# Performance work log

Measured on AMD Instinct MI355X. Metric: run time of the kernel, lower is better.

The kernel has to match this reference:

```python
import jax, jax.numpy as jnp
import numpy as np

IMG = 12
SIZE = 100000
ACC_SCALE = 255.0     # accurate_dft scale
APX_SCALE = 65536.0   # mod_scale for mult index 1 (in {1,2,4,10,11})


def _dft_mat():
    # scipy.linalg.dft(12): W[j,k] = exp(-2*pi*i*j*k/12); module adds 1e-5
    j = np.arange(IMG)
    W = np.exp(-2j * np.pi * np.outer(j, j) / IMG)
    return W.real + 1e-5, W.imag + 1e-5


def setup_inputs() -> dict:
    key = jax.random.key(0)
    x = jax.random.uniform(key, (1, SIZE, IMG, IMG), dtype=jnp.float32) * 255.0
    re, im = _dft_mat()
    wr = jnp.asarray(re.reshape(1, IMG * IMG), dtype=jnp.float32)
    wi = jnp.asarray(im.reshape(1, IMG * IMG), dtype=jnp.float32)
    return {"input": x, "weight_real": wr, "weight_imag": wi}


def _dft_pass(wr_flat, wi_flat, x, scale, rounded):
    # x: (size, 12, 12); wr_flat/wi_flat: (144,)
    rw = wr_flat.reshape(IMG, IMG)
    iw = wi_flat.reshape(IMG, IMG)
    if rounded:  # approx_dft quantizes weights to integers in [-(scale-1), scale-1]
        rw = jnp.round(rw * (scale - 1.0))
        iw = jnp.round(iw * (scale - 1.0))
    else:        # accurate_dft just scales
        rw = rw * scale
        iw = iw * scale
    # approx_matmul's tile/elementwise-mul/group-sum is exactly W @ x[i] per batch
    rt = jnp.matmul(rw, x) / scale          # (size,12,12)
    it = jnp.matmul(iw, x) / scale
    ro = (jnp.matmul(rt, rw) - jnp.matmul(it, iw)) / scale
    io = (jnp.matmul(rt, iw) + jnp.matmul(it, rw)) / scale
    return jnp.sqrt(ro * ro + io * io)      # |re + i*im|


def reference(input, weight_real, weight_imag):
    x = input[:, :, :IMG, :IMG][0]  # (size,12,12)
    acc = _dft_pass(weight_real[0], weight_imag[0], x, ACC_SCALE, False)
    apx = _dft_pass(weight_real[0], weight_imag[0], x, APX_SCALE, True)
    # torch `x.data = x_data` -> straight-through: value = approx, grad via accurate
    out = acc + jax.lax.stop_gradient(apx - acc)
    # output layout [len(mult_list)=1, 1, size, 12, 12]
    return out[None, None]
```

## Files before the change

### kernel.cpp

```cpp
#include <hip/hip_runtime.h>

#define IMG  12
#define NPIX 144
#define IPB  21
#define XSTR 148
#define THREADS 256

__device__ __forceinline__ float rfl(float v) {
    return __builtin_bit_cast(float, __builtin_amdgcn_readfirstlane(__builtin_bit_cast(int, v)));
}

__global__ __launch_bounds__(THREADS)
void dft_apx_kernel(const float* __restrict__ x,
                    const float* __restrict__ wr,
                    const float* __restrict__ wi,
                    float* __restrict__ out, int size)
{
    __shared__ float bufA[IPB * XSTR];
    __shared__ float bufB[IPB * XSTR];

    const int tid  = threadIdx.x;
    const int img0 = blockIdx.x * IPB;
    int nimg = size - img0; if (nimg > IPB) nimg = IPB;

    float cq[12], sq[12];
    #pragma unroll
    for (int m = 0; m < 12; ++m) {
        cq[m] = rfl(rintf(wr[12 + m] * 65535.0f));
        sq[m] = rfl(rintf(wi[12 + m] * 65535.0f));
    }

    const float4* xg = (const float4*)(x + (size_t)img0 * NPIX);
    const int n4 = nimg * (NPIX / 4);
    for (int i = tid; i < n4; i += THREADS) {
        const int im = i / 36, e4 = i % 36;
        *(float4*)&bufA[im * XSTR + e4 * 4] = xg[i];
    }
    __syncthreads();

    const int img_l  = tid / IMG;
    const int lane12 = tid - img_l * IMG;
    const bool active = (tid < IPB * IMG) && (img_l < nimg);

    float xr[12];
    if (active) {
        #pragma unroll
        for (int j = 0; j < 12; ++j)
            xr[j] = bufA[img_l * XSTR + j * IMG + lane12];
    }
    __syncthreads();

    if (active) {
        #pragma unroll
        for (int r = 0; r < 12; ++r) {
            float ar = 0.0f, ai = 0.0f;
            #pragma unroll
            for (int j = 0; j < 12; ++j) {
                const int m = (r * j) % 12;
                ar = fmaf(cq[m], xr[j], ar);
                ai = fmaf(sq[m], xr[j], ai);
            }
            bufA[img_l * XSTR + r * IMG + lane12] = ar;
            bufB[img_l * XSTR + r * IMG + lane12] = ai;
        }
    }
    __syncthreads();

    if (active) {
        float rt[12], it[12];
        #pragma unroll
        for (int q = 0; q < 3; ++q) {
            float4 a = *(const float4*)&bufA[img_l * XSTR + lane12 * IMG + q * 4];
            float4 b = *(const float4*)&bufB[img_l * XSTR + lane12 * IMG + q * 4];
            rt[q*4+0]=a.x; rt[q*4+1]=a.y; rt[q*4+2]=a.z; rt[q*4+3]=a.w;
            it[q*4+0]=b.x; it[q*4+1]=b.y; it[q*4+2]=b.z; it[q*4+3]=b.w;
        }
        const float inv32 = 2.3283064365386963e-10f;
        float o[12];
        #pragma unroll
        for (int cc = 0; cc < 12; ++cc) {
            float ro = 0.0f, io = 0.0f;
            #pragma unroll
            for (int j = 0; j < 12; ++j) {
                const int m = (j * cc) % 12;
                ro = fmaf(rt[j],  cq[m], ro);
                ro = fmaf(-it[j], sq[m], ro);
                io = fmaf(rt[j],  sq[m], io);
                io = fmaf(it[j],  cq[m], io);
            }
            o[cc] = __builtin_amdgcn_sqrtf(fmaf(ro, ro, io * io)) * inv32;
        }
        float4* og = (float4*)(out + (size_t)(img0 + img_l) * NPIX + lane12 * IMG);
        og[0] = make_float4(o[0], o[1], o[2],  o[3]);
        og[1] = make_float4(o[4], o[5], o[6],  o[7]);
        og[2] = make_float4(o[8], o[9], o[10], o[11]);
    }
}

extern "C" void kernel_launch(void* const* d_in, const int* in_sizes, int n_in,
                              void* d_out, int out_size, void* d_ws, size_t ws_size,
                              hipStream_t stream) {
    const float* x  = (const float*)d_in[0];
    const float* wr = (const float*)d_in[1];
    const float* wi = (const float*)d_in[2];
    float* out = (float*)d_out;

    const int size = in_sizes[0] / NPIX;
    const int blocks = (size + IPB - 1) / IPB;
    dft_apx_kernel<<<blocks, THREADS, 0, stream>>>(x, wr, wi, out, size);
}
```

Measured before the change: 125.0 us.

## Map one image per thread with register-held input and shared weight table

Changes the work decomposition from 12 threads per image with LDS transposes to one thread per image. Each thread holds the whole 144-float image in registers and computes each output row directly. The quantized, index-permuted weights go into a small shared table read as float4 broadcasts. This removes the LDS staging buffers and the intermediate barriers, but needs a very large register footprint per thread, and each thread's float4 loads are strided 576 bytes from its neighbours, so global accesses are poorly coalesced.

```diff
diff --git a/kernel.cpp b/kernel.cpp
--- a/kernel.cpp
+++ b/kernel.cpp
@@ -2,98 +2,89 @@
 
 #define IMG  12
 #define NPIX 144
-#define IPB  21
-#define XSTR 148
-#define THREADS 256
+#define THREADS 64
 
 __device__ __forceinline__ float rfl(float v) {
     return __builtin_bit_cast(float, __builtin_amdgcn_readfirstlane(__builtin_bit_cast(int, v)));
 }
 
-__global__ __launch_bounds__(THREADS)
+__global__ __launch_bounds__(THREADS, 2)
 void dft_apx_kernel(const float* __restrict__ x,
                     const float* __restrict__ wr,
                     const float* __restrict__ wi,
                     float* __restrict__ out, int size)
 {
-    __shared__ float bufA[IPB * XSTR];
-    __shared__ float bufB[IPB * XSTR];
+    __shared__ float wqc[NPIX], wqs[NPIX];
 
-    const int tid  = threadIdx.x;
-    const int img0 = blockIdx.x * IPB;
-    int nimg = size - img0; if (nimg > IPB) nimg = IPB;
+    const int tid = threadIdx.x;
+    for (int t = tid; t < NPIX; t += THREADS) {
+        const int r = t / IMG, j = t - r * IMG;
+        const int m = (r * j) % IMG;
+        wqc[t] = rintf(wr[IMG + m] * 65535.0f);
+        wqs[t] = rintf(wi[IMG + m] * 65535.0f);
+    }
+    __syncthreads();
 
     float cq[12], sq[12];
     #pragma unroll
     for (int m = 0; m < 12; ++m) {
-        cq[m] = rfl(rintf(wr[12 + m] * 65535.0f));
-        sq[m] = rfl(rintf(wi[12 + m] * 65535.0f));
+        cq[m] = rfl(rintf(wr[IMG + m] * 65535.0f));
+        sq[m] = rfl(rintf(wi[IMG + m] * 65535.0f));
     }
 
-    const float4* xg = (const float4*)(x + (size_t)img0 * NPIX);
-    const int n4 = nimg * (NPIX / 4);
-    for (int i = tid; i < n4; i += THREADS) {
-        const int im = i / 36, e4 = i % 36;
-        *(float4*)&bufA[im * XSTR + e4 * 4] = xg[i];
+    const int img = blockIdx.x * THREADS + tid;
+    if (img >= size) return;
+
+    float X[NPIX];
+    const float4* xg = (const float4*)(x + (size_t)img * NPIX);
+    #pragma unroll
+    for (int k = 0; k < NPIX / 4; ++k) {
+        const float4 v = xg[k];
+        X[4*k+0] = v.x; X[4*k+1] = v.y; X[4*k+2] = v.z; X[4*k+3] = v.w;
     }
-    __syncthreads();
 
-    const int img_l  = tid / IMG;
-    const int lane12 = tid - img_l * IMG;
-    const bool active = (tid < IPB * IMG) && (img_l < nimg);
+    float* og = out + (size_t)img * NPIX;
+    const float inv32 = 2.3283064365386963e-10f;
 
-    float xr[12];
-    if (active) {
+    #pragma unroll 1
+    for (int r = 0; r < IMG; ++r) {
+        float cr[12], sr[12];
         #pragma unroll
-        for (int j = 0; j < 12; ++j)
-            xr[j] = bufA[img_l * XSTR + j * IMG + lane12];
-    }
-    __syncthreads();
-
-    if (active) {
+        for (int q = 0; q < 3; ++q) {
+            const float4 a = *(const float4*)&wqc[r * IMG + 4*q];
+            const float4 b = *(const float4*)&wqs[r * IMG + 4*q];
+            cr[4*q+0]=a.x; cr[4*q+1]=a.y; cr[4*q+2]=a.z; cr[4*q+3]=a.w;
+            sr[4*q+0]=b.x; sr[4*q+1]=b.y; sr[4*q+2]=b.z; sr[4*q+3]=b.w;
+        }
+        float rt[12], it[12];
         #pragma unroll
-        for (int r = 0; r < 12; ++r) {
-            float ar = 0.0f, ai = 0.0f;
+        for (int c = 0; c < 12; ++c) {
+            float a = 0.0f, b = 0.0f;
             #pragma unroll
             for (int j = 0; j < 12; ++j) {
-                const int m = (r * j) % 12;
-                ar = fmaf(cq[m], xr[j], ar);
-                ai = fmaf(sq[m], xr[j], ai);
+                a = fmaf(cr[j], X[j*12 + c], a);
+                b = fmaf(sr[j], X[j*12 + c], b);
             }
-            bufA[img_l * XSTR + r * IMG + lane12] = ar;
-            bufB[img_l * XSTR + r * IMG + lane12] = ai;
+            rt[c] = a; it[c] = b;
         }
-    }
-    __syncthreads();
-
-    if (active) {
-        float rt[12], it[12];
-        #pragma unroll
-        for (int q = 0; q < 3; ++q) {
-            float4 a = *(const float4*)&bufA[img_l * XSTR + lane12 * IMG + q * 4];
-            float4 b = *(const float4*)&bufB[img_l * XSTR + lane12 * IMG + q * 4];
-            rt[q*4+0]=a.x; rt[q*4+1]=a.y; rt[q*4+2]=a.z; rt[q*4+3]=a.w;
-            it[q*4+0]=b.x; it[q*4+1]=b.y; it[q*4+2]=b.z; it[q*4+3]=b.w;
-        }
-        const float inv32 = 2.3283064365386963e-10f;
         float o[12];
         #pragma unroll
-        for (int cc = 0; cc < 12; ++cc) {
+        for (int c = 0; c < 12; ++c) {
             float ro = 0.0f, io = 0.0f;
             #pragma unroll
             for (int j = 0; j < 12; ++j) {
-                const int m = (j * cc) % 12;
+                const int m = (j * c) % 12;
                 ro = fmaf(rt[j],  cq[m], ro);
                 ro = fmaf(-it[j], sq[m], ro);
                 io = fmaf(rt[j],  sq[m], io);
                 io = fmaf(it[j],  cq[m], io);
             }
-            o[cc] = __builtin_amdgcn_sqrtf(fmaf(ro, ro, io * io)) * inv32;
+            o[c] = __builtin_amdgcn_sqrtf(fmaf(ro, ro, io * io)) * inv32;
         }
-        float4* og = (float4*)(out + (size_t)(img0 + img_l) * NPIX + lane12 * IMG);
-        og[0] = make_float4(o[0], o[1], o[2],  o[3]);
-        og[1] = make_float4(o[4], o[5], o[6],  o[7]);
-        og[2] = make_float4(o[8], o[9], o[10], o[11]);
+        float4* orow = (float4*)(og + r * IMG);
+        orow[0] = make_float4(o[0], o[1], o[2],  o[3]);
+        orow[1] = make_float4(o[4], o[5], o[6],  o[7]);
+        orow[2] = make_float4(o[8], o[9], o[10], o[11]);
     }
 }
 
@@ -106,6 +97,6 @@
     float* out = (float*)d_out;
 
     const int size = in_sizes[0] / NPIX;
-    const int blocks = (size + IPB - 1) / IPB;
+    const int blocks = (size + THREADS - 1) / THREADS;
     dft_apx_kernel<<<blocks, THREADS, 0, stream>>>(x, wr, wi, out, size);
 }
```

New measurement: 131.1 us. +4.9%, slower.
